# Optimization experiments

Hardware: AMD Instinct MI355X
Metric: run time of the kernel (lower is better)

The kernel has to match this reference:

```python
import jax, jax.numpy as jnp
import numpy as np

HEADS = 8


def setup_inputs() -> dict:
    key = jax.random.key(0)
    ks = jax.random.split(key, 6)
    dim = 256
    s = 0.02
    return {
        "x": jax.random.normal(ks[0], (8, dim, 32, 32), jnp.float32),
        "w_qkv": jax.random.normal(ks[1], (3 * dim, dim), jnp.float32) * s,
        "w_out": jax.random.normal(ks[2], (dim, dim), jnp.float32) * s,
        "b_out": jnp.zeros((dim,), jnp.float32),
        "w_g1": jax.random.normal(ks[3], (dim // 4, dim), jnp.float32) * s,
        "b_g1": jnp.zeros((dim // 4,), jnp.float32),
        "w_g2": jax.random.normal(ks[4], (1, dim // 4), jnp.float32) * s,
        "b_g2": jnp.zeros((1,), jnp.float32),
    }


def _conv1x1(t, w, bias=None):
    # 1x1 conv == channel matmul
    y = jnp.einsum('bchw,oc->bohw', t, w)
    if bias is not None:
        y = y + bias[None, :, None, None]
    return y


def _forward(x, w_qkv, w_out, b_out, w_g1, b_g1, w_g2, b_g2):
    b, c, h, w = x.shape
    heads = HEADS
    d = c // heads
    n = h * w
    m = min(h, w)
    scale = d ** (-0.5)

    qkv = _conv1x1(x, w_qkv)  # [b, 3c, h, w]

    def to_heads(t):  # 'b (h d) x y -> b h (x y) d'
        return t.reshape(b, heads, d, n).transpose(0, 1, 3, 2)

    q, k, v = (to_heads(t) for t in jnp.split(qkv, 3, axis=1))

    attn = jax.nn.softmax(jnp.einsum('bhid,bhjd->bhij', q, k) * scale, axis=-1)

    # diagonal branch (anti-diagonal scores are computed in the original but
    # never used in the output -> omitted as dead code)
    q2d = q.reshape(b, heads, h, w, d)
    k2d = k.reshape(b, heads, h, w, d)
    q_dm = jnp.diagonal(q2d, axis1=2, axis2=3)  # [b, heads, d, m]
    k_dm = jnp.diagonal(k2d, axis1=2, axis2=3)
    diag_main = jnp.einsum('bhnd,bhmd->bhnm', q_dm, k_dm) * scale  # [b, heads, d, d]
    diag_vec = jnp.diagonal(diag_main.mean(axis=1), axis1=-2, axis2=-1)  # [b, d]
    diag_vec = jnp.pad(diag_vec, ((0, 0), (0, n - m)))  # [b, n] (d == m)

    DIAG_WEIGHT = 0.3
    enhanced = attn + DIAG_WEIGHT * diag_vec[:, None, :, None]

    out = jnp.einsum('bhij,bhjd->bhid', enhanced, v)  # [b, heads, n, d]
    out = out.reshape(b, heads, h, w, d).transpose(0, 1, 4, 2, 3).reshape(b, c, h, w)

    # left/right asymmetry gate
    mid = w // 2
    left = x[:, :, :, :mid]
    right = x[:, :, :, mid:]
    asym = jnp.abs(left - right[:, :, :, ::-1])  # [b, c, h, w/2]
    # adaptive_avg_pool2d (h, w/2) -> (h, w) with even w == width repeat by 2
    pooled = jnp.repeat(asym, 2, axis=3)
    g = _conv1x1(pooled, w_g1, b_g1)
    g = jax.nn.gelu(g, approximate=False)
    g = jax.nn.sigmoid(_conv1x1(g, w_g2, b_g2))  # [b, 1, h, w]

    out = out * (1.0 + g)
    return _conv1x1(out, w_out, b_out)


def reference(x, w_qkv, w_out, b_out, w_g1, b_g1, w_g2, b_g2):
    return _forward(x, w_qkv, w_out, b_out, w_g1, b_g1, w_g2, b_g2)
```

## Files before the change

### kernel.cpp

```cpp
#include <hip/hip_runtime.h>
#include <hip/hip_bf16.h>
#include <math.h>

#define B 8
#define C 256
#define HEADS 8
#define D 32
#define NPIX 1024
#define OC 768
#define SCALE 0.17677669529663687f
#define LOG2E 1.4426950408889634f

typedef unsigned int uint;
typedef unsigned short u16;
typedef __attribute__((ext_vector_type(8))) short bf16x8;
typedef __attribute__((ext_vector_type(4))) short bf16x4;
typedef __attribute__((ext_vector_type(4))) float f32x4;

static __device__ inline u16 f2bf(float f) {
  uint u = __float_as_uint(f);
  return (u16)((u + 0x7fffu + ((u >> 16) & 1u)) >> 16);
}
static __device__ inline float bf_lo(uint u) { return __uint_as_float(u << 16); }
static __device__ inline float bf_hi(uint u) { return __uint_as_float(u & 0xffff0000u); }

static __device__ inline uint pk2(float lo, float hi) {
  union { __hip_bfloat162 h; uint u; } cv;
  cv.h = __float22bfloat162_rn(float2{lo, hi});
  return cv.u;
}

__global__ __launch_bounds__(256) void k_prep(
    const float* __restrict__ x, const float* __restrict__ wqkv,
    const float* __restrict__ wout,
    u16* __restrict__ WQ, u16* __restrict__ WO, u16* __restrict__ XT) {
  const int bid = blockIdx.x, t = threadIdx.x;
  __shared__ u16 tile[64][65];
  if (bid < 256) {
    const float* src;
    u16* dst;
    int base;
    if (bid < 192) { src = wqkv; dst = WQ; base = bid * 1024; }
    else           { src = wout; dst = WO; base = (bid - 192) * 1024; }
    float4 v = *(const float4*)(src + base + t * 4);
    uint2 pk = make_uint2((uint)f2bf(v.x) | ((uint)f2bf(v.y) << 16),
                          (uint)f2bf(v.z) | ((uint)f2bf(v.w) << 16));
    *(uint2*)(dst + base + t * 4) = pk;
    return;
  }
  const int id = bid - 256;
  const int pt = id & 15, ct = (id >> 4) & 3, b = id >> 6;
  {
    const int px = t & 63, cq = t >> 6;
    const float* xb = x + ((size_t)(b * C + ct * 64)) * NPIX + pt * 64;
#pragma unroll
    for (int m = 0; m < 16; ++m) {
      const int c = cq * 16 + m;
      tile[c][px] = f2bf(xb[(size_t)c * NPIX + px]);
    }
  }
  __syncthreads();
  {
    const int cc = t & 63, pq = t >> 6;
    u16* dst = XT + ((size_t)(b * NPIX + pt * 64)) * C + ct * 64;
#pragma unroll
    for (int m = 0; m < 16; ++m) {
      const int pix = pq * 16 + m;
      dst[(size_t)pix * C + cc] = tile[cc][pix];
    }
  }
}

__global__ __launch_bounds__(256) void k_qkv_mfma(
    const u16* __restrict__ XT, const u16* __restrict__ WQ,
    u16* __restrict__ Q, u16* __restrict__ Kk, u16* __restrict__ VT) {
  const int ob = blockIdx.x, pb = blockIdx.y, b = blockIdx.z;
  const int wv = threadIdx.x >> 6, lane = threadIdx.x & 63;
  const int quad = lane >> 4, l15 = lane & 15;
  const int part = ob >> 2;
  const int odl = (ob & 3) * 64 + wv * 16;
  const int hh = odl >> 5, d0 = odl & 31;
  const int bh = b * HEADS + hh;
  const int pix0 = pb * 128;

  const u16* arow = WQ + (size_t)(ob * 64 + wv * 16 + l15) * C;
  bf16x8 af[8];
#pragma unroll
  for (int kc = 0; kc < 8; ++kc)
    af[kc] = *(const bf16x8*)(arow + kc * 32 + quad * 8);

  const u16* xb = XT + (size_t)(b * NPIX + pix0) * C;
  f32x4 acc[8];
#pragma unroll
  for (int nt = 0; nt < 8; ++nt) acc[nt] = (f32x4){0.f, 0.f, 0.f, 0.f};

  for (int kc = 0; kc < 8; ++kc) {
#pragma unroll
    for (int nt = 0; nt < 8; ++nt) {
      bf16x8 bfr = *(const bf16x8*)(xb + (size_t)(nt * 16 + l15) * C +
                                    kc * 32 + quad * 8);
      acc[nt] = __builtin_amdgcn_mfma_f32_16x16x32_bf16(af[kc], bfr, acc[nt], 0, 0, 0);
    }
  }

  if (part < 2) {
    const float qs = (part == 0) ? (SCALE * LOG2E) : 1.f;
    u16* dst = (part == 0 ? Q : Kk) + (size_t)bh * NPIX * D;
#pragma unroll
    for (int nt = 0; nt < 8; ++nt) {
      const int pix = pix0 + nt * 16 + l15;
      uint2 pk = make_uint2(
          (uint)f2bf(acc[nt][0] * qs) | ((uint)f2bf(acc[nt][1] * qs) << 16),
          (uint)f2bf(acc[nt][2] * qs) | ((uint)f2bf(acc[nt][3] * qs) << 16));
      *(uint2*)(dst + (size_t)pix * D + d0 + 4 * quad) = pk;
    }
  } else {
    u16* vb = VT + (size_t)bh * NPIX * D;
#pragma unroll
    for (int nt = 0; nt < 8; ++nt) {
      const int pix = pix0 + nt * 16 + l15;
      const int jb16 = pix >> 4, qa = (pix >> 2) & 3, m = pix & 3;
#pragma unroll
      for (int r = 0; r < 4; ++r) {
        const int d = d0 + 4 * quad + r;
        const int nta = d >> 4, l15a = d & 15;
        vb[((size_t)(jb16 * 2 + nta) * 64 + qa * 16 + l15a) * 4 + m] =
            f2bf(acc[nt][r]);
      }
    }
  }
}

__global__ __launch_bounds__(256) void k_red(
    const uint* __restrict__ Q, const uint* __restrict__ Kk,
    const u16* __restrict__ VT, float* __restrict__ diagv,
    float* __restrict__ colsum) {
  const int bid = blockIdx.x, tid = threadIdx.x;
  __shared__ float red[256];
  if (bid < 8) {
    const int b = bid;
    const int hh = tid >> 5, dd = tid & 31;
    const uint* qb = Q + (size_t)(b * HEADS + hh) * NPIX * (D / 2);
    const uint* kb = Kk + (size_t)(b * HEADS + hh) * NPIX * (D / 2);
    float s = 0.f;
#pragma unroll 4
    for (int t = 0; t < 32; ++t) {
      uint qu = qb[t * 33 * (D / 2) + dd / 2];
      uint ku = kb[t * 33 * (D / 2) + dd / 2];
      float qv = (dd & 1) ? bf_hi(qu) : bf_lo(qu);
      float kv = (dd & 1) ? bf_hi(ku) : bf_lo(ku);
      s += qv * kv;
    }
    red[tid] = s;
    __syncthreads();
    if (tid < 32) {
      float v = 0.f;
#pragma unroll
      for (int h8 = 0; h8 < 8; ++h8) v += red[h8 * 32 + tid];
      diagv[b * 32 + tid] = v * (0.125f / LOG2E);
    }
  } else {
    const int bh = bid - 8;
    const int d = tid >> 3, sl = tid & 7;
    const int nta = d >> 4, l15a = d & 15;
    const u16* vb = VT + (size_t)bh * NPIX * D;
    float s = 0.f;
    for (int jb = 0; jb < 8; ++jb) {
      const int jb16 = sl * 8 + jb;
#pragma unroll
      for (int qa = 0; qa < 4; ++qa) {
        const uint2 u = *(const uint2*)(
            vb + ((size_t)(jb16 * 2 + nta) * 64 + qa * 16 + l15a) * 4);
        s += bf_lo(u.x) + bf_hi(u.x) + bf_lo(u.y) + bf_hi(u.y);
      }
    }
    red[tid] = s;
    __syncthreads();
    if (tid < 32) {
      float v = 0.f;
#pragma unroll
      for (int g = 0; g < 8; ++g) v += red[tid * 8 + g];
      colsum[bh * D + tid] = v;
    }
  }
}

__global__ __launch_bounds__(256, 4) void k_attn(
    const u16* __restrict__ Q, const u16* __restrict__ Kk,
    const u16* __restrict__ VT, const float* __restrict__ diagv,
    const float* __restrict__ colsum, u16* __restrict__ AOT) {
  const int qc = blockIdx.x;
  const int bh = blockIdx.y;
  const int b = bh >> 3, hh = bh & 7;
  const int wv = threadIdx.x >> 6, lane = threadIdx.x & 63;
  const int quad = lane >> 4, l15 = lane & 15;
  const int i0 = qc * 64 + wv * 16;

  const u16* Qb  = Q  + (size_t)bh * NPIX * D;
  const u16* Kb  = Kk + (size_t)bh * NPIX * D;
  const u16* VFb = VT + (size_t)bh * NPIX * D;

  bf16x8 qfrag = *(const bf16x8*)(Qb + (size_t)(i0 + l15) * D + quad * 8);

  f32x4 oacc[2];
  oacc[0] = (f32x4){0.f, 0.f, 0.f, 0.f};
  oacc[1] = (f32x4){0.f, 0.f, 0.f, 0.f};
  float lacc[4] = {};

  const u16* kp  = Kb + (size_t)l15 * D + quad * 8;
  const u16* vfp = VFb + (size_t)lane * 4;

  for (int it = 0; it < 16; ++it) {
    bf16x4 vf[4][2];
#pragma unroll
    for (int jt = 0; jt < 4; ++jt)
#pragma unroll
      for (int nt = 0; nt < 2; ++nt)
        vf[jt][nt] = *(const bf16x4*)(
            vfp + (size_t)(((it * 4 + jt) * 2 + nt) * 256));

    f32x4 st[4];
#pragma unroll
    for (int jt = 0; jt < 4; ++jt) {
      bf16x8 kfrag = *(const bf16x8*)(kp + (size_t)(it * 64 + jt * 16) * D);
      st[jt] = __builtin_amdgcn_mfma_f32_16x16x32_bf16(
          kfrag, qfrag, (f32x4){0.f, 0.f, 0.f, 0.f}, 0, 0, 0);
    }

#pragma unroll
    for (int jt = 0; jt < 4; ++jt)
#pragma unroll
      for (int r = 0; r < 4; ++r) {
        float pv = exp2f(fminf(st[jt][r], 80.f));
        lacc[r] += pv;
        st[jt][r] = pv;
      }

    __builtin_amdgcn_s_setprio(1);
#pragma unroll
    for (int jt = 0; jt < 4; ++jt) {
      union { uint u[2]; bf16x4 v; } pa;
      pa.u[0] = pk2(st[jt][0], st[jt][1]);
      pa.u[1] = pk2(st[jt][2], st[jt][3]);
#pragma unroll
      for (int nt = 0; nt < 2; ++nt)
        oacc[nt] = __builtin_amdgcn_mfma_f32_16x16x16bf16_1k(
            pa.v, vf[jt][nt], oacc[nt], 0, 0, 0);
    }
    __builtin_amdgcn_s_setprio(0);
  }

  float lt = (lacc[0] + lacc[1]) + (lacc[2] + lacc[3]);
  lt += __shfl_xor(lt, 16, 64);
  lt += __shfl_xor(lt, 32, 64);
  const float linv = 1.f / lt;
  float rinv[4];
#pragma unroll
  for (int r = 0; r < 4; ++r) rinv[r] = __shfl(linv, quad * 4 + r, 64);

  const bool do_diag = (i0 < 32);
#pragma unroll
  for (int nt = 0; nt < 2; ++nt) {
    const int dch = hh * 32 + nt * 16 + l15;
    float cs = do_diag ? colsum[bh * D + (nt * 16 + l15)] : 0.f;
#pragma unroll
    for (int r = 0; r < 4; ++r) {
      const int irow = i0 + quad * 4 + r;
      float o = oacc[nt][r] * rinv[r];
      if (do_diag) o += 0.3f * diagv[b * 32 + irow] * cs;
      AOT[((size_t)b * NPIX + irow) * C + dch] = f2bf(o);
    }
  }
}

__global__ __launch_bounds__(256) void k_gate(
    const float* __restrict__ x,
    const float* __restrict__ wg1, const float* __restrict__ bg1,
    const float* __restrict__ wg2, const float* __restrict__ bg2,
    float* __restrict__ gate) {
  const int h = blockIdx.x, b = blockIdx.y, tid = threadIdx.x;
  __shared__ float pl[16 * 257];
  __shared__ float gl[16 * 65];

  {
    const int c = tid;
    const float* row = x + ((size_t)(b * C + c) * NPIX + h * 32);
    float v[32];
#pragma unroll
    for (int m = 0; m < 32; ++m) v[m] = row[m];
#pragma unroll
    for (int k = 0; k < 16; ++k) pl[k * 257 + c] = fabsf(v[k] - v[31 - k]);
  }
  __syncthreads();

  const int o16 = tid >> 4, k = tid & 15;
#pragma unroll 1
  for (int p = 0; p < 4; ++p) {
    const int o = p * 16 + o16;
    const float* wr = wg1 + o * C;
    float a0 = 0.f, a1 = 0.f, a2 = 0.f, a3 = 0.f;
#pragma unroll 4
    for (int c = 0; c < C; c += 4) {
      a0 += wr[c]     * pl[k * 257 + c];
      a1 += wr[c + 1] * pl[k * 257 + c + 1];
      a2 += wr[c + 2] * pl[k * 257 + c + 2];
      a3 += wr[c + 3] * pl[k * 257 + c + 3];
    }
    float a = bg1[o] + ((a0 + a1) + (a2 + a3));
    gl[k * 65 + o] = 0.5f * a * (1.f + erff(a * 0.70710678118654752f));
  }
  __syncthreads();

  if (tid < 16) {
    float s = bg2[0];
    for (int o = 0; o < 64; ++o)
      s += wg2[o] * gl[tid * 65 + o];
    gate[(b * 32 + h) * 16 + tid] = 1.f / (1.f + expf(-s));
  }
}

__global__ __launch_bounds__(256) void k_out_mfma(
    const u16* __restrict__ AOT, const u16* __restrict__ WO,
    const float* __restrict__ bout, const float* __restrict__ gate,
    float* __restrict__ out) {
  const int ob = blockIdx.x, pb = blockIdx.y, b = blockIdx.z;
  const int wv = threadIdx.x >> 6, lane = threadIdx.x & 63;
  const int quad = lane >> 4, l15 = lane & 15;
  const int o0 = ob * 64 + wv * 16;
  const int pix0 = pb * 128;

  const u16* arow = WO + (size_t)(o0 + l15) * C;
  bf16x8 af[8];
#pragma unroll
  for (int kc = 0; kc < 8; ++kc)
    af[kc] = *(const bf16x8*)(arow + kc * 32 + quad * 8);

  const u16* ab = AOT + (size_t)(b * NPIX + pix0) * C;
  f32x4 acc[8];
#pragma unroll
  for (int nt = 0; nt < 8; ++nt) acc[nt] = (f32x4){0.f, 0.f, 0.f, 0.f};

  for (int kc = 0; kc < 8; ++kc) {
#pragma unroll
    for (int nt = 0; nt < 8; ++nt) {
      bf16x8 bfr = *(const bf16x8*)(ab + (size_t)(nt * 16 + l15) * C +
                                    kc * 32 + quad * 8);
      acc[nt] = __builtin_amdgcn_mfma_f32_16x16x32_bf16(af[kc], bfr, acc[nt], 0, 0, 0);
    }
  }

#pragma unroll
  for (int nt = 0; nt < 8; ++nt) {
    const int pix = pix0 + nt * 16 + l15;
    const float gf = 1.f + gate[(b * 32 + (pix >> 5)) * 16 + ((pix & 31) >> 1)];
#pragma unroll
    for (int r = 0; r < 4; ++r) {
      const int o = o0 + 4 * quad + r;
      out[((size_t)b * C + o) * NPIX + pix] = acc[nt][r] * gf + bout[o];
    }
  }
}

extern "C" void kernel_launch(void* const* d_in, const int* in_sizes, int n_in,
                              void* d_out, int out_size, void* d_ws, size_t ws_size,
                              hipStream_t stream) {
  const float* x    = (const float*)d_in[0];
  const float* wqkv = (const float*)d_in[1];
  const float* wout = (const float*)d_in[2];
  const float* bout = (const float*)d_in[3];
  const float* wg1  = (const float*)d_in[4];
  const float* bg1  = (const float*)d_in[5];
  const float* wg2  = (const float*)d_in[6];
  const float* bg2  = (const float*)d_in[7];
  float* out = (float*)d_out;

  const size_t SZ = (size_t)B * HEADS * NPIX * D;
  u16* XT = (u16*)d_ws;
  u16* WQ = XT + SZ;
  u16* WO = WQ + (size_t)OC * C;
  u16* Q  = WO + (size_t)C * C;
  u16* Kq = Q + SZ;
  u16* VT = Kq + SZ;
  float* DIAG = (float*)(VT + SZ);
  float* COL  = DIAG + 256;
  float* GATE = COL + 2048;
  u16* AOT = XT;

  hipLaunchKernelGGL(k_prep, dim3(768), dim3(256), 0, stream,
                     x, wqkv, wout, WQ, WO, XT);
  hipLaunchKernelGGL(k_qkv_mfma, dim3(12, 8, B), dim3(256), 0, stream,
                     XT, WQ, Q, Kq, VT);
  hipLaunchKernelGGL(k_red, dim3(72), dim3(256), 0, stream,
                     (const uint*)Q, (const uint*)Kq, VT, DIAG, COL);
  hipLaunchKernelGGL(k_attn, dim3(16, 64), dim3(256), 0, stream,
                     Q, Kq, VT, DIAG, COL, AOT);
  hipLaunchKernelGGL(k_gate, dim3(32, B), dim3(256), 0, stream,
                     x, wg1, bg1, wg2, bg2, GATE);
  hipLaunchKernelGGL(k_out_mfma, dim3(4, 8, B), dim3(256), 0, stream,
                     AOT, WO, bout, GATE, out);
}
```

Baseline: 171.6 us.

## Stage K and V tiles in shared memory with double buffering in attention

The QKV kernel now writes K in an MFMA-fragment-ordered layout, so each 64-key tile is a contiguous 2048-element chunk. The attention kernel has all four waves cooperatively load the K and V tiles into double-buffered LDS, then read fragments from LDS. Before, each wave loaded the same K/V fragments straight from global memory. This cuts redundant global and L2 traffic, at the cost of a block-wide barrier every iteration and 16 KB of LDS per block, which may reduce occupancy. The diagonal reduction kernel is updated to index the new K layout.

```diff
diff --git a/kernel.cpp b/kernel.cpp
--- a/kernel.cpp
+++ b/kernel.cpp
@@ -21,6 +21,7 @@
   uint u = __float_as_uint(f);
   return (u16)((u + 0x7fffu + ((u >> 16) & 1u)) >> 16);
 }
+static __device__ inline float bfval(u16 v) { return __uint_as_float((uint)v << 16); }
 static __device__ inline float bf_lo(uint u) { return __uint_as_float(u << 16); }
 static __device__ inline float bf_hi(uint u) { return __uint_as_float(u & 0xffff0000u); }
 
@@ -103,9 +104,9 @@
     }
   }
 
-  if (part < 2) {
-    const float qs = (part == 0) ? (SCALE * LOG2E) : 1.f;
-    u16* dst = (part == 0 ? Q : Kk) + (size_t)bh * NPIX * D;
+  if (part == 0) {
+    const float qs = SCALE * LOG2E;
+    u16* dst = Q + (size_t)bh * NPIX * D;
 #pragma unroll
     for (int nt = 0; nt < 8; ++nt) {
       const int pix = pix0 + nt * 16 + l15;
@@ -114,6 +115,16 @@
           (uint)f2bf(acc[nt][2] * qs) | ((uint)f2bf(acc[nt][3] * qs) << 16));
       *(uint2*)(dst + (size_t)pix * D + d0 + 4 * quad) = pk;
     }
+  } else if (part == 1) {
+    u16* kfb = Kk + (size_t)bh * NPIX * D;
+    const int lane_k8 = (((d0 >> 3) + (quad >> 1)) * 16 + l15) * 8 + (quad & 1) * 4;
+#pragma unroll
+    for (int nt = 0; nt < 8; ++nt) {
+      uint2 pk = make_uint2(
+          (uint)f2bf(acc[nt][0]) | ((uint)f2bf(acc[nt][1]) << 16),
+          (uint)f2bf(acc[nt][2]) | ((uint)f2bf(acc[nt][3]) << 16));
+      *(uint2*)(kfb + (size_t)(pb * 8 + nt) * 512 + lane_k8) = pk;
+    }
   } else {
     u16* vb = VT + (size_t)bh * NPIX * D;
 #pragma unroll
@@ -132,7 +143,7 @@
 }
 
 __global__ __launch_bounds__(256) void k_red(
-    const uint* __restrict__ Q, const uint* __restrict__ Kk,
+    const u16* __restrict__ Q, const u16* __restrict__ KF,
     const u16* __restrict__ VT, float* __restrict__ diagv,
     float* __restrict__ colsum) {
   const int bid = blockIdx.x, tid = threadIdx.x;
@@ -140,15 +151,15 @@
   if (bid < 8) {
     const int b = bid;
     const int hh = tid >> 5, dd = tid & 31;
-    const uint* qb = Q + (size_t)(b * HEADS + hh) * NPIX * (D / 2);
-    const uint* kb = Kk + (size_t)(b * HEADS + hh) * NPIX * (D / 2);
+    const u16* qb = Q + (size_t)(b * HEADS + hh) * NPIX * D;
+    const u16* kb = KF + (size_t)(b * HEADS + hh) * NPIX * D;
     float s = 0.f;
 #pragma unroll 4
     for (int t = 0; t < 32; ++t) {
-      uint qu = qb[t * 33 * (D / 2) + dd / 2];
-      uint ku = kb[t * 33 * (D / 2) + dd / 2];
-      float qv = (dd & 1) ? bf_hi(qu) : bf_lo(qu);
-      float kv = (dd & 1) ? bf_hi(ku) : bf_lo(ku);
+      const int j = t * 33;
+      float qv = bfval(qb[(size_t)j * D + dd]);
+      float kv = bfval(kb[(size_t)(j >> 4) * 512 +
+                          ((dd >> 3) * 16 + (j & 15)) * 8 + (dd & 7)]);
       s += qv * kv;
     }
     red[tid] = s;
@@ -186,8 +197,8 @@
 }
 
 __global__ __launch_bounds__(256, 4) void k_attn(
-    const u16* __restrict__ Q, const u16* __restrict__ Kk,
-    const u16* __restrict__ VT, const float* __restrict__ diagv,
+    const u16* __restrict__ Q, const u16* __restrict__ KF,
+    const u16* __restrict__ VF, const float* __restrict__ diagv,
     const float* __restrict__ colsum, u16* __restrict__ AOT) {
   const int qc = blockIdx.x;
   const int bh = blockIdx.y;
@@ -196,9 +207,11 @@
   const int quad = lane >> 4, l15 = lane & 15;
   const int i0 = qc * 64 + wv * 16;
 
+  __shared__ u16 sbuf[2][4096];
+
   const u16* Qb  = Q  + (size_t)bh * NPIX * D;
-  const u16* Kb  = Kk + (size_t)bh * NPIX * D;
-  const u16* VFb = VT + (size_t)bh * NPIX * D;
+  const u16* KFb = KF + (size_t)bh * NPIX * D;
+  const u16* VFb = VF + (size_t)bh * NPIX * D;
 
   bf16x8 qfrag = *(const bf16x8*)(Qb + (size_t)(i0 + l15) * D + quad * 8);
 
@@ -207,22 +220,34 @@
   oacc[1] = (f32x4){0.f, 0.f, 0.f, 0.f};
   float lacc[4] = {};
 
-  const u16* kp  = Kb + (size_t)l15 * D + quad * 8;
-  const u16* vfp = VFb + (size_t)lane * 4;
-
+  const u16* gsrc = (wv < 2 ? KFb : VFb) + (wv & 1) * 1024 + lane * 8;
+  u16* ldst[2] = { &sbuf[0][wv * 1024 + lane * 8],
+                   &sbuf[1][wv * 1024 + lane * 8] };
+
+  {
+    uint4 a = *(const uint4*)(gsrc);
+    uint4 c = *(const uint4*)(gsrc + 512);
+    *(uint4*)(ldst[0]) = a;
+    *(uint4*)(ldst[0] + 512) = c;
+  }
+  __syncthreads();
+
+  int cur = 0;
   for (int it = 0; it < 16; ++it) {
-    bf16x4 vf[4][2];
-#pragma unroll
-    for (int jt = 0; jt < 4; ++jt)
-#pragma unroll
-      for (int nt = 0; nt < 2; ++nt)
-        vf[jt][nt] = *(const bf16x4*)(
-            vfp + (size_t)(((it * 4 + jt) * 2 + nt) * 256));
+    if (it < 15) {
+      uint4 a = *(const uint4*)(gsrc + (size_t)(it + 1) * 2048);
+      uint4 c = *(const uint4*)(gsrc + (size_t)(it + 1) * 2048 + 512);
+      u16* ld = ldst[cur ^ 1];
+      *(uint4*)(ld) = a;
+      *(uint4*)(ld + 512) = c;
+    }
+    const u16* sK = &sbuf[cur][0];
+    const u16* sV = &sbuf[cur][2048];
 
     f32x4 st[4];
 #pragma unroll
     for (int jt = 0; jt < 4; ++jt) {
-      bf16x8 kfrag = *(const bf16x8*)(kp + (size_t)(it * 64 + jt * 16) * D);
+      bf16x8 kfrag = *(const bf16x8*)(sK + jt * 512 + lane * 8);
       st[jt] = __builtin_amdgcn_mfma_f32_16x16x32_bf16(
           kfrag, qfrag, (f32x4){0.f, 0.f, 0.f, 0.f}, 0, 0, 0);
     }
@@ -243,11 +268,16 @@
       pa.u[0] = pk2(st[jt][0], st[jt][1]);
       pa.u[1] = pk2(st[jt][2], st[jt][3]);
 #pragma unroll
-      for (int nt = 0; nt < 2; ++nt)
+      for (int nt = 0; nt < 2; ++nt) {
+        bf16x4 vfr = *(const bf16x4*)(sV + (jt * 2 + nt) * 256 + lane * 4);
         oacc[nt] = __builtin_amdgcn_mfma_f32_16x16x16bf16_1k(
-            pa.v, vf[jt][nt], oacc[nt], 0, 0, 0);
+            pa.v, vfr, oacc[nt], 0, 0, 0);
+      }
     }
     __builtin_amdgcn_s_setprio(0);
+
+    __syncthreads();
+    cur ^= 1;
   }
 
   float lt = (lacc[0] + lacc[1]) + (lacc[2] + lacc[3]);
@@ -391,7 +421,7 @@
   hipLaunchKernelGGL(k_qkv_mfma, dim3(12, 8, B), dim3(256), 0, stream,
                      XT, WQ, Q, Kq, VT);
   hipLaunchKernelGGL(k_red, dim3(72), dim3(256), 0, stream,
-                     (const uint*)Q, (const uint*)Kq, VT, DIAG, COL);
+                     Q, Kq, VT, DIAG, COL);
   hipLaunchKernelGGL(k_attn, dim3(16, 64), dim3(256), 0, stream,
                      Q, Kq, VT, DIAG, COL, AOT);
   hipLaunchKernelGGL(k_gate, dim3(32, B), dim3(256), 0, stream,
```

Result: no change. 169.0 us (-1.5%).
